# Optimization experiments

Measured on AMD Instinct MI355X. Metric: run time of the kernel, lower is better.

The kernel has to match this reference:

```python
import jax, jax.numpy as jnp
import numpy as np

OFFSETS = jnp.array([[-1, -1], [0, -1], [1, -1], [-1, 0], [0, 0], [1, 0],
                     [-1, 1], [0, 1], [1, 1]], dtype=jnp.float32)  # [9,2]
PIX_STEP = 2.0 / 96.0


def _bilinear_sample(img, gx, gy):
    """Bilinear grid_sample, padding_mode='zeros', align_corners=False.
    img: [B,H,W]; gx, gy: [B,P] in normalized coords [-1,1]. Returns [B,P]."""
    B, H, W = img.shape
    ix = ((gx + 1.0) * W - 1.0) * 0.5  # x indexes width
    iy = ((gy + 1.0) * H - 1.0) * 0.5
    x0f = jnp.floor(ix)
    y0f = jnp.floor(iy)
    wx = ix - x0f
    wy = iy - y0f
    x0 = x0f.astype(jnp.int32)
    y0 = y0f.astype(jnp.int32)
    x1 = x0 + 1
    y1 = y0 + 1
    flat = img.reshape(B, H * W)

    def gather(xi, yi):
        valid = (xi >= 0) & (xi < W) & (yi >= 0) & (yi < H)
        xc = jnp.clip(xi, 0, W - 1)
        yc = jnp.clip(yi, 0, H - 1)
        vals = jnp.take_along_axis(flat, yc * W + xc, axis=1)
        return jnp.where(valid, vals, 0.0)

    v00 = gather(x0, y0)
    v10 = gather(x1, y0)
    v01 = gather(x0, y1)
    v11 = gather(x1, y1)
    return (v00 * (1 - wx) * (1 - wy) + v10 * wx * (1 - wy)
            + v01 * (1 - wx) * wy + v11 * wx * wy)


def setup_inputs() -> dict:
    key = jax.random.key(0)
    k1, k2, k3 = jax.random.split(key, 3)
    B, N, H, W = 256, 16384, 96, 96
    corners = jax.random.uniform(k1, (B, N, 2), dtype=jnp.float32)
    edge_map = jax.random.uniform(k2, (B, 1, H, W), dtype=jnp.float32)
    mask_map = jax.random.uniform(k3, (B, 1, H, W), dtype=jnp.float32)
    return {"corners": corners, "edge_map": edge_map, "mask_map": mask_map}


def reference(corners, edge_map, mask_map):
    B, N, _ = corners.shape
    grid = corners * 2.0 - 1.0  # [B,N,2] (x,y)
    # 9-point neighborhood around each corner: [B,N,9,2]
    neigh = grid[:, :, None, :] + OFFSETS[None, None] * PIX_STEP
    gx = neigh[..., 0].reshape(B, N * 9)
    gy = neigh[..., 1].reshape(B, N * 9)
    sampled_edges = _bilinear_sample(edge_map[:, 0], gx, gy).reshape(B, N, 9)
    best_edge = jnp.max(sampled_edges, axis=-1)  # [B,N]
    edge_align_loss = jnp.mean(1.0 - best_edge)
    sampled_mask = _bilinear_sample(mask_map[:, 0], grid[..., 0], grid[..., 1])  # [B,N]
    mask_align_loss = jnp.mean((sampled_mask - 0.5) ** 2)
    return edge_align_loss + 2.0 * mask_align_loss
```

## Files before the change

### kernel.cpp

```cpp
#include <hip/hip_runtime.h>
#include <hip/hip_fp16.h>

constexpr int Bn = 256;
constexpr int Nn = 16384;
constexpr int Hh = 96;
constexpr int Ww = 96;

constexpr int THREADS = 1024;
constexpr int CHUNKS  = 2;

constexpr int MOFF = 10000;
constexpr int TOTENT = 19800;

static __device__ inline float2 up2(__half2 h) { return __half22float2(h); }

#define ADDR(sfx, CX, CY)                                                   \
    float ix##sfx = fmaf(CX, 96.f, -0.5f);                                  \
    float iy##sfx = fmaf(CY, 96.f, -0.5f);                                  \
    float fx##sfx = floorf(ix##sfx), fy##sfx = floorf(iy##sfx);             \
    float wx##sfx = ix##sfx - fx##sfx, wy##sfx = iy##sfx - fy##sfx;         \
    int v##sfx  = (int)fy##sfx * 100 + (int)fx##sfx;                        \
    int cb##sfx = v##sfx + 101;                                             \
    int c3##sfx = v##sfx + 401;                                             \
    int mb##sfx = v##sfx + MOFF + 102;

#define ISSUE(sfx)                                                          \
    __half2 a0##sfx = sB[cb##sfx],       d0##sfx = sB[cb##sfx + 2];         \
    __half2 a1##sfx = sB[cb##sfx + 100], d1##sfx = sB[cb##sfx + 102];       \
    __half2 a2##sfx = sB[cb##sfx + 200], d2##sfx = sB[cb##sfx + 202];       \
    __half2 a3##sfx = sB[c3##sfx],       d3##sfx = sB[c3##sfx + 2];         \
    __half2 ma##sfx = sB[mb##sfx],       mc##sfx = sB[mb##sfx + 100];

#define COMPUTE(sfx)                                                        \
    {                                                                       \
        float2 A0 = up2(a0##sfx), D0 = up2(d0##sfx);                        \
        float2 A1 = up2(a1##sfx), D1 = up2(d1##sfx);                        \
        float2 A2 = up2(a2##sfx), D2 = up2(d2##sfx);                        \
        float2 A3 = up2(a3##sfx), D3 = up2(d3##sfx);                        \
        float wx = wx##sfx, wy = wy##sfx;                                   \
        float h00 = fmaf(wx, A0.y - A0.x, A0.x);                            \
        float h01 = fmaf(wx, D0.x - A0.y, A0.y);                            \
        float h02 = fmaf(wx, D0.y - D0.x, D0.x);                            \
        float h10 = fmaf(wx, A1.y - A1.x, A1.x);                            \
        float h11 = fmaf(wx, D1.x - A1.y, A1.y);                            \
        float h12 = fmaf(wx, D1.y - D1.x, D1.x);                            \
        float h20 = fmaf(wx, A2.y - A2.x, A2.x);                            \
        float h21 = fmaf(wx, D2.x - A2.y, A2.y);                            \
        float h22 = fmaf(wx, D2.y - D2.x, D2.x);                            \
        float h30 = fmaf(wx, A3.y - A3.x, A3.x);                            \
        float h31 = fmaf(wx, D3.x - A3.y, A3.y);                            \
        float h32 = fmaf(wx, D3.y - D3.x, D3.x);                            \
        float v00 = fmaf(wy, h10 - h00, h00);                               \
        float v01 = fmaf(wy, h11 - h01, h01);                               \
        float v02 = fmaf(wy, h12 - h02, h02);                               \
        float v10 = fmaf(wy, h20 - h10, h10);                               \
        float v11 = fmaf(wy, h21 - h11, h11);                               \
        float v12 = fmaf(wy, h22 - h12, h12);                               \
        float v20 = fmaf(wy, h30 - h20, h20);                               \
        float v21 = fmaf(wy, h31 - h21, h21);                               \
        float v22 = fmaf(wy, h32 - h22, h22);                               \
        float best = fmaxf(fmaxf(fmaxf(v00, v01), fmaxf(v02, v10)),         \
                           fmaxf(fmaxf(v11, v12),                           \
                                 fmaxf(fmaxf(v20, v21), v22)));             \
        eAcc += best;                                                       \
        float2 qa = up2(ma##sfx), qc = up2(mc##sfx);                        \
        float t = fmaf(wx, qa.y - qa.x, qa.x);                              \
        float u = fmaf(wx, qc.y - qc.x, qc.x);                              \
        float m = fmaf(wy, u - t, t);                                       \
        float d = m - 0.5f;                                                 \
        mAcc = fmaf(d, d, mAcc);                                            \
    }

__global__ __launch_bounds__(THREADS, 8)
void geo_kernel(const float* __restrict__ corners,
                const float* __restrict__ edge,
                const float* __restrict__ mask,
                float2* __restrict__ partial)
{
    __shared__ __half2 sB[TOTENT];
    __shared__ float redE[THREADS / 64];
    __shared__ float redM[THREADS / 64];

    const int b     = blockIdx.x >> 1;
    const int chunk = blockIdx.x & 1;
    const int tid   = threadIdx.x;

    {
        const __half2 z2 = __halves2half2(__ushort_as_half(0), __ushort_as_half(0));
        for (int i = tid; i < 1176; i += THREADS) {
            int idx;
            if (i < 200)        idx = i;
            else if (i < 400)   idx = 9600 + i;
            else if (i < 500)   idx = MOFF + (i - 400);
            else if (i < 600)   idx = MOFF + 9200 + i;
            else if (i < 888) { int k = i - 600; int r = k / 3; int c3 = k - 3 * r;
                                int c = (c3 == 0) ? 0 : (97 + c3);
                                idx = (r + 2) * 100 + c; }
            else              { int k = i - 888; int r = k / 3; int c3 = k - 3 * r;
                                int c = (c3 == 0) ? 0 : (97 + c3);
                                idx = MOFF + (r + 1) * 100 + c; }
            sB[idx] = z2;
        }
    }

    {
        const float* ebase = edge + (size_t)b * Hh * Ww;
        const float* mbase = mask + (size_t)b * Hh * Ww;
        for (int i = tid; i < 96 * 48; i += THREADS) {
            int r = i / 48;
            int j = i - 48 * r;
            const float* erow = ebase + r * Ww;
            const float* mrow = mbase + r * Ww;
            float2 ae = *(const float2*)(erow + 2 * j);
            float2 am = *(const float2*)(mrow + 2 * j);
            float ne = (2 * j + 2 < Ww) ? erow[2 * j + 2] : 0.f;
            float nm = (2 * j + 2 < Ww) ? mrow[2 * j + 2] : 0.f;
            int eb2 = (r + 2) * 100 + 2 * j + 2;
            sB[eb2]     = __float22half2_rn(make_float2(ae.x, ae.y));
            sB[eb2 + 1] = __float22half2_rn(make_float2(ae.y, ne));
            int mb2 = MOFF + (r + 1) * 100 + 2 * j + 2;
            sB[mb2]     = __float22half2_rn(make_float2(am.x, am.y));
            sB[mb2 + 1] = __float22half2_rn(make_float2(am.y, nm));
            if (j == 0) {
                sB[(r + 2) * 100 + 1]        = __float22half2_rn(make_float2(0.f, ae.x));
                sB[MOFF + (r + 1) * 100 + 1] = __float22half2_rn(make_float2(0.f, am.x));
            }
        }
    }
    __syncthreads();

    const float4* c4 =
        (const float4*)(corners + (size_t)b * Nn * 2 + (size_t)chunk * (Nn / CHUNKS) * 2);
    float eAcc = 0.f, mAcc = 0.f;

    float4 nxt = c4[tid];
#pragma unroll
    for (int k = 0; k < 4; ++k) {
        float4 cur = nxt;
        if (k < 3) nxt = c4[(k + 1) * THREADS + tid];

        ADDR(A, cur.x, cur.y)
        ISSUE(A)
        ADDR(B, cur.z, cur.w)
        ISSUE(B)
        COMPUTE(A)
        COMPUTE(B)
    }

#pragma unroll
    for (int off = 32; off > 0; off >>= 1) {
        eAcc += __shfl_xor(eAcc, off);
        mAcc += __shfl_xor(mAcc, off);
    }
    const int wv = tid >> 6;
    const int ln = tid & 63;
    if (ln == 0) { redE[wv] = eAcc; redM[wv] = mAcc; }
    __syncthreads();

    if (tid == 0) {
        float e = 0.f, m = 0.f;
#pragma unroll
        for (int w = 0; w < THREADS / 64; ++w) { e += redE[w]; m += redM[w]; }
        partial[blockIdx.x] = make_float2(e, m);
    }
}

__global__ __launch_bounds__(512)
void geo_reduce(const float2* __restrict__ partial, float* __restrict__ out)
{
    __shared__ double rE[8];
    __shared__ double rM[8];
    const int tid = threadIdx.x;
    float2 p = partial[tid];
    double e = (double)p.x, m = (double)p.y;
#pragma unroll
    for (int off = 32; off > 0; off >>= 1) {
        e += __shfl_xor(e, off);
        m += __shfl_xor(m, off);
    }
    if ((tid & 63) == 0) { rE[tid >> 6] = e; rM[tid >> 6] = m; }
    __syncthreads();
    if (tid == 0) {
        double se = 0.0, sm = 0.0;
#pragma unroll
        for (int w = 0; w < 8; ++w) { se += rE[w]; sm += rM[w]; }
        const double inv = 1.0 / (double)((long long)Bn * (long long)Nn);
        double edge_loss = 1.0 - se * inv;
        double mask_loss = sm * inv;
        out[0] = (float)(edge_loss + 2.0 * mask_loss);
    }
}

extern "C" void kernel_launch(void* const* d_in, const int* in_sizes, int n_in,
                              void* d_out, int out_size, void* d_ws, size_t ws_size,
                              hipStream_t stream)
{
    const float* corners = (const float*)d_in[0];
    const float* edge    = (const float*)d_in[1];
    const float* mask    = (const float*)d_in[2];
    float* out      = (float*)d_out;
    float2* partial = (float2*)d_ws;

    geo_kernel<<<Bn * CHUNKS, THREADS, 0, stream>>>(corners, edge, mask, partial);
    geo_reduce<<<1, 512, 0, stream>>>(partial, out);
}
```

Baseline: 25.31 us.

## Fuse final reduction via last-block atomic counter and software-pipeline LDS gathers

Replaces the separate single-block reduce kernel with a last-block-done pattern: each block publishes its partial, bumps an atomic counter, and the final block sums all partials in double and writes the loss. The main loop is also restructured so the shared-memory gathers for the next corner pair are issued before the current pair's interpolation finishes, which overlaps LDS latency with arithmetic. The second kernel launch is traded for a memset launch plus a fence and atomic per block, and the longer live ranges may raise register pressure.

```diff
diff --git a/kernel.cpp b/kernel.cpp
--- a/kernel.cpp
+++ b/kernel.cpp
@@ -14,30 +14,33 @@
 
 static __device__ inline float2 up2(__half2 h) { return __half22float2(h); }
 
-#define ADDR(sfx, CX, CY)                                                   \
-    float ix##sfx = fmaf(CX, 96.f, -0.5f);                                  \
-    float iy##sfx = fmaf(CY, 96.f, -0.5f);                                  \
-    float fx##sfx = floorf(ix##sfx), fy##sfx = floorf(iy##sfx);             \
-    float wx##sfx = ix##sfx - fx##sfx, wy##sfx = iy##sfx - fy##sfx;         \
-    int v##sfx  = (int)fy##sfx * 100 + (int)fx##sfx;                        \
-    int cb##sfx = v##sfx + 101;                                             \
-    int c3##sfx = v##sfx + 401;                                             \
-    int mb##sfx = v##sfx + MOFF + 102;
-
-#define ISSUE(sfx)                                                          \
-    __half2 a0##sfx = sB[cb##sfx],       d0##sfx = sB[cb##sfx + 2];         \
-    __half2 a1##sfx = sB[cb##sfx + 100], d1##sfx = sB[cb##sfx + 102];       \
-    __half2 a2##sfx = sB[cb##sfx + 200], d2##sfx = sB[cb##sfx + 202];       \
-    __half2 a3##sfx = sB[c3##sfx],       d3##sfx = sB[c3##sfx + 2];         \
-    __half2 ma##sfx = sB[mb##sfx],       mc##sfx = sB[mb##sfx + 100];
-
-#define COMPUTE(sfx)                                                        \
+#define DECLSET(s)                                                          \
+    float wx##s, wy##s; int cb##s, c3##s, mb##s;                            \
+    __half2 a0##s, d0##s, a1##s, d1##s, a2##s, d2##s, a3##s, d3##s,         \
+            ma##s, mc##s;
+
+#define ADDRW(s, CX, CY) {                                                  \
+    float ix = fmaf(CX, 96.f, -0.5f);                                       \
+    float iy = fmaf(CY, 96.f, -0.5f);                                       \
+    float fx = floorf(ix), fy = floorf(iy);                                 \
+    wx##s = ix - fx; wy##s = iy - fy;                                       \
+    int v = (int)fy * 100 + (int)fx;                                        \
+    cb##s = v + 101; c3##s = v + 401; mb##s = v + MOFF + 102; }
+
+#define ISSUEW(s)                                                           \
+    a0##s = sB[cb##s];       d0##s = sB[cb##s + 2];                         \
+    a1##s = sB[cb##s + 100]; d1##s = sB[cb##s + 102];                       \
+    a2##s = sB[cb##s + 200]; d2##s = sB[cb##s + 202];                       \
+    a3##s = sB[c3##s];       d3##s = sB[c3##s + 2];                         \
+    ma##s = sB[mb##s];       mc##s = sB[mb##s + 100];
+
+#define COMPUTE(s)                                                          \
     {                                                                       \
-        float2 A0 = up2(a0##sfx), D0 = up2(d0##sfx);                        \
-        float2 A1 = up2(a1##sfx), D1 = up2(d1##sfx);                        \
-        float2 A2 = up2(a2##sfx), D2 = up2(d2##sfx);                        \
-        float2 A3 = up2(a3##sfx), D3 = up2(d3##sfx);                        \
-        float wx = wx##sfx, wy = wy##sfx;                                   \
+        float2 A0 = up2(a0##s), D0 = up2(d0##s);                            \
+        float2 A1 = up2(a1##s), D1 = up2(d1##s);                            \
+        float2 A2 = up2(a2##s), D2 = up2(d2##s);                            \
+        float2 A3 = up2(a3##s), D3 = up2(d3##s);                            \
+        float wx = wx##s, wy = wy##s;                                       \
         float h00 = fmaf(wx, A0.y - A0.x, A0.x);                            \
         float h01 = fmaf(wx, D0.x - A0.y, A0.y);                            \
         float h02 = fmaf(wx, D0.y - D0.x, D0.x);                            \
@@ -63,7 +66,7 @@
                            fmaxf(fmaxf(v11, v12),                           \
                                  fmaxf(fmaxf(v20, v21), v22)));             \
         eAcc += best;                                                       \
-        float2 qa = up2(ma##sfx), qc = up2(mc##sfx);                        \
+        float2 qa = up2(ma##s), qc = up2(mc##s);                            \
         float t = fmaf(wx, qa.y - qa.x, qa.x);                              \
         float u = fmaf(wx, qc.y - qc.x, qc.x);                              \
         float m = fmaf(wy, u - t, t);                                       \
@@ -75,11 +78,16 @@
 void geo_kernel(const float* __restrict__ corners,
                 const float* __restrict__ edge,
                 const float* __restrict__ mask,
-                float2* __restrict__ partial)
+                float2* __restrict__ partial,
+                unsigned* __restrict__ cnt,
+                float* __restrict__ out)
 {
     __shared__ __half2 sB[TOTENT];
-    __shared__ float redE[THREADS / 64];
-    __shared__ float redM[THREADS / 64];
+    __shared__ float  redE[THREADS / 64];
+    __shared__ float  redM[THREADS / 64];
+    __shared__ double rDE[8];
+    __shared__ double rDM[8];
+    __shared__ unsigned isLast;
 
     const int b     = blockIdx.x >> 1;
     const int chunk = blockIdx.x & 1;
@@ -133,17 +141,24 @@
         (const float4*)(corners + (size_t)b * Nn * 2 + (size_t)chunk * (Nn / CHUNKS) * 2);
     float eAcc = 0.f, mAcc = 0.f;
 
+    DECLSET(A)
+    DECLSET(B)
+
     float4 nxt = c4[tid];
+    float4 cur = nxt;
+    ADDRW(A, cur.x, cur.y)
+    ISSUEW(A)
 #pragma unroll
     for (int k = 0; k < 4; ++k) {
-        float4 cur = nxt;
+        cur = nxt;
         if (k < 3) nxt = c4[(k + 1) * THREADS + tid];
-
-        ADDR(A, cur.x, cur.y)
-        ISSUE(A)
-        ADDR(B, cur.z, cur.w)
-        ISSUE(B)
+        ADDRW(B, cur.z, cur.w)
+        ISSUEW(B)
         COMPUTE(A)
+        if (k < 3) {
+            ADDRW(A, nxt.x, nxt.y)
+            ISSUEW(A)
+        }
         COMPUTE(B)
     }
 
@@ -162,32 +177,36 @@
 #pragma unroll
         for (int w = 0; w < THREADS / 64; ++w) { e += redE[w]; m += redM[w]; }
         partial[blockIdx.x] = make_float2(e, m);
-    }
-}
-
-__global__ __launch_bounds__(512)
-void geo_reduce(const float2* __restrict__ partial, float* __restrict__ out)
-{
-    __shared__ double rE[8];
-    __shared__ double rM[8];
-    const int tid = threadIdx.x;
-    float2 p = partial[tid];
-    double e = (double)p.x, m = (double)p.y;
-#pragma unroll
-    for (int off = 32; off > 0; off >>= 1) {
-        e += __shfl_xor(e, off);
-        m += __shfl_xor(m, off);
-    }
-    if ((tid & 63) == 0) { rE[tid >> 6] = e; rM[tid >> 6] = m; }
+        __threadfence();
+        unsigned old = atomicAdd(cnt, 1u);
+        isLast = (old == (unsigned)(gridDim.x - 1)) ? 1u : 0u;
+    }
     __syncthreads();
-    if (tid == 0) {
-        double se = 0.0, sm = 0.0;
-#pragma unroll
-        for (int w = 0; w < 8; ++w) { se += rE[w]; sm += rM[w]; }
-        const double inv = 1.0 / (double)((long long)Bn * (long long)Nn);
-        double edge_loss = 1.0 - se * inv;
-        double mask_loss = sm * inv;
-        out[0] = (float)(edge_loss + 2.0 * mask_loss);
+
+    if (isLast) {
+        double e = 0.0, m = 0.0;
+        if (tid < 512) {
+            float pe = atomicAdd(&((float*)partial)[2 * tid + 0], 0.f);
+            float pm = atomicAdd(&((float*)partial)[2 * tid + 1], 0.f);
+            e = (double)pe;
+            m = (double)pm;
+        }
+#pragma unroll
+        for (int off = 32; off > 0; off >>= 1) {
+            e += __shfl_xor(e, off);
+            m += __shfl_xor(m, off);
+        }
+        if (tid < 512 && ln == 0) { rDE[wv] = e; rDM[wv] = m; }
+        __syncthreads();
+        if (tid == 0) {
+            double se = 0.0, sm = 0.0;
+#pragma unroll
+            for (int w = 0; w < 8; ++w) { se += rDE[w]; sm += rDM[w]; }
+            const double inv = 1.0 / (double)((long long)Bn * (long long)Nn);
+            double edge_loss = 1.0 - se * inv;
+            double mask_loss = sm * inv;
+            out[0] = (float)(edge_loss + 2.0 * mask_loss);
+        }
     }
 }
 
@@ -200,7 +219,9 @@
     const float* mask    = (const float*)d_in[2];
     float* out      = (float*)d_out;
     float2* partial = (float2*)d_ws;
-
-    geo_kernel<<<Bn * CHUNKS, THREADS, 0, stream>>>(corners, edge, mask, partial);
-    geo_reduce<<<1, 512, 0, stream>>>(partial, out);
+    unsigned* cnt   = (unsigned*)((char*)d_ws + 512 * sizeof(float2));
+
+    hipMemsetAsync(cnt, 0, sizeof(unsigned), stream);
+    geo_kernel<<<Bn * CHUNKS, THREADS, 0, stream>>>(corners, edge, mask,
+                                                    partial, cnt, out);
 }
```

Result: slower. 35.25 us (+39.3%).
